# Performance work log

Hardware: AMD Instinct MI355X
Metric: run time of the kernel (lower is better)

## Reference

```python
import jax, jax.numpy as jnp
import numpy as np

N_NODES = 50000


def _mlp(h, W1, b1, W2, b2):
    return jax.nn.relu(h @ W1.T + b1) @ W2.T + b2


def _gine_layer(h, src, dst, e_emb):
    # messages: ReLU(x_src + edge_embedding), summed at destination (PyG GINEConv, eps=0)
    m = jax.nn.relu(h[src] + e_emb)                       # [E, D]
    agg = jax.ops.segment_sum(m, dst, num_segments=N_NODES)
    return h + agg                                         # (1+eps)*x + agg, eps=0


def setup_inputs() -> dict:
    key = jax.random.key(0)
    ks = jax.random.split(key, 20)
    N, E = N_NODES, 800000
    in_dim, hid, edim, n_types = 64, 128, 16, 100
    s = 0.05
    inp = {
        "x": jax.random.normal(ks[0], (N, in_dim), jnp.float32),
        "edge_index": jax.random.randint(ks[1], (2, E), 0, N, jnp.int64),
        "edge_attr": jax.random.normal(ks[2], (E, edim), jnp.float32),
        "edge_weights": jax.random.uniform(ks[3], (E,), jnp.float32),
        # layer 1: edge lin edim->in_dim, node MLP in_dim->hid->hid
        "We1": jax.random.normal(ks[4], (in_dim, edim), jnp.float32) * s,
        "be1": jnp.zeros((in_dim,), jnp.float32),
        "W11": jax.random.normal(ks[5], (hid, in_dim), jnp.float32) * s,
        "b11": jnp.zeros((hid,), jnp.float32),
        "W12": jax.random.normal(ks[6], (hid, hid), jnp.float32) * s,
        "b12": jnp.zeros((hid,), jnp.float32),
        # layer 2: edge lin edim->hid, node MLP hid->hid->hid
        "We2": jax.random.normal(ks[7], (hid, edim), jnp.float32) * s,
        "be2": jnp.zeros((hid,), jnp.float32),
        "W21": jax.random.normal(ks[8], (hid, hid), jnp.float32) * s,
        "b21": jnp.zeros((hid,), jnp.float32),
        "W22": jax.random.normal(ks[9], (hid, hid), jnp.float32) * s,
        "b22": jnp.zeros((hid,), jnp.float32),
        # output head hid -> n_atom_types
        "Wo": jax.random.normal(ks[10], (n_types, hid), jnp.float32) * s,
        "bo": jnp.zeros((n_types,), jnp.float32),
    }
    return inp


def reference(x, edge_index, edge_attr, edge_weights,
              We1, be1, W11, b11, W12, b12,
              We2, be2, W21, b21, W22, b22,
              Wo, bo):
    src, dst = edge_index[0], edge_index[1]
    ea = edge_attr * edge_weights[:, None]                 # per-edge scaling
    # layer 1
    h = _gine_layer(x, src, dst, ea @ We1.T + be1)
    h = jax.nn.relu(_mlp(h, W11, b11, W12, b12))
    # layer 2
    h = _gine_layer(h, src, dst, ea @ We2.T + be2)
    h = jax.nn.relu(_mlp(h, W21, b21, W22, b22))
    return h @ Wo.T + bo
```

## Files before the change

### kernel.cpp

```cpp
#include <hip/hip_runtime.h>

#define N_NODES 50000
#define E_EDGES 800000
#define SCAN_NB 196

__global__ __launch_bounds__(256) void k_hist(
    const int* __restrict__ ei, int* __restrict__ cnt)
{
    const int e = blockIdx.x * 256 + threadIdx.x;
    if (e < E_EDGES) atomicAdd(&cnt[ei[E_EDGES + e]], 1);
}

__global__ __launch_bounds__(256) void k_scan1(
    const int* __restrict__ cnt, int* __restrict__ bsum)
{
    __shared__ int red[256];
    const int tid = threadIdx.x;
    const int i = blockIdx.x * 256 + tid;
    red[tid] = (i < N_NODES) ? cnt[i] : 0;
    __syncthreads();
    for (int off = 128; off > 0; off >>= 1) {
        if (tid < off) red[tid] += red[tid + off];
        __syncthreads();
    }
    if (tid == 0) bsum[blockIdx.x] = red[0];
}

__global__ __launch_bounds__(256) void k_scan2(
    const int* __restrict__ bsum, int* __restrict__ boff)
{
    __shared__ int part[256];
    const int tid = threadIdx.x;
    const int v = (tid < SCAN_NB) ? bsum[tid] : 0;
    part[tid] = v;
    __syncthreads();
    for (int off = 1; off < 256; off <<= 1) {
        const int vv = part[tid];
        const int u = (tid >= off) ? part[tid - off] : 0;
        __syncthreads();
        part[tid] = vv + u;
        __syncthreads();
    }
    if (tid < SCAN_NB) boff[tid] = part[tid] - v;
}

__global__ __launch_bounds__(256) void k_scan3(
    const int* __restrict__ cnt, const int* __restrict__ boff,
    int* __restrict__ rowptr, int* __restrict__ cursor)
{
    __shared__ int part[256];
    const int tid = threadIdx.x;
    const int i = blockIdx.x * 256 + tid;
    const int v = (i < N_NODES) ? cnt[i] : 0;
    part[tid] = v;
    __syncthreads();
    for (int off = 1; off < 256; off <<= 1) {
        const int vv = part[tid];
        const int u = (tid >= off) ? part[tid - off] : 0;
        __syncthreads();
        part[tid] = vv + u;
        __syncthreads();
    }
    const int excl = part[tid] - v + boff[blockIdx.x];
    if (i < N_NODES) { rowptr[i] = excl; cursor[i] = excl; }
    if (i == N_NODES) rowptr[N_NODES] = excl;
}

__global__ __launch_bounds__(256) void k_scatter(
    const int* __restrict__ ei, int* __restrict__ cursor, int2* __restrict__ pairs)
{
    const int e = blockIdx.x * 256 + threadIdx.x;
    if (e < E_EDGES) {
        const int dst = ei[E_EDGES + e];
        const int pos = atomicAdd(&cursor[dst], 1);
        pairs[pos] = make_int2(ei[e], e);
    }
}

__global__ __launch_bounds__(256) void k_prep(
    const int2* __restrict__ pairs, const float* __restrict__ eattr,
    const float* __restrict__ ew, float* __restrict__ eaw, int* __restrict__ srcs)
{
    const int t = blockIdx.x * 256 + threadIdx.x;
    const int pos = t >> 2;
    if (pos >= E_EDGES) return;
    const int q = t & 3;
    const int2 p = pairs[pos];
    if (q == 0) srcs[pos] = p.x;
    const float w = ew[p.y];
    const float4 a = *((const float4*)(eattr + (size_t)p.y * 16) + q);
    *((float4*)(eaw + (size_t)pos * 16) + q) =
        make_float4(a.x * w, a.y * w, a.z * w, a.w * w);
}

__global__ __launch_bounds__(256) void k_wt(
    const float* __restrict__ W11, const float* __restrict__ W12,
    const float* __restrict__ W21, const float* __restrict__ W22,
    const float* __restrict__ Wo,
    const float* __restrict__ We1, const float* __restrict__ We2,
    float* __restrict__ WT)
{
    const int bid = blockIdx.x;
    const int tid = threadIdx.x;
    if (bid < 288) {
        const float* src; int KIN, JOUT, lbase, obase;
        if (bid < 32)       { src = W11; KIN = 64;  JOUT = 128; lbase = 0;   obase = 0; }
        else if (bid < 96)  { src = W12; KIN = 128; JOUT = 128; lbase = 32;  obase = 8192; }
        else if (bid < 160) { src = W21; KIN = 128; JOUT = 128; lbase = 96;  obase = 24576; }
        else if (bid < 224) { src = W22; KIN = 128; JOUT = 128; lbase = 160; obase = 40960; }
        else                { src = Wo;  KIN = 128; JOUT = 100; lbase = 224; obase = 57344; }
        const int idx = (bid - lbase) * 256 + tid;
        const int k = idx >> 7, j = idx & 127;
        WT[obase + idx] = (j < JOUT) ? src[j * KIN + k] : 0.f;
    } else if (bid < 292) {
        const int idx = (bid - 288) * 256 + tid;
        const int k = idx >> 6, d = idx & 63;
        WT[73728 + idx] = We1[d * 16 + k];
    } else {
        const int idx = (bid - 292) * 256 + tid;
        const int k = idx >> 7, d = idx & 127;
        WT[74752 + idx] = We2[d * 16 + k];
    }
}

__global__ __launch_bounds__(256, 4) void k_edge1(
    const int* __restrict__ rp, const int* __restrict__ srcs,
    const float* __restrict__ eaw,
    const float* __restrict__ WeT1, const float* __restrict__ be1,
    const float* __restrict__ x, float* __restrict__ out)
{
    const int lane = threadIdx.x & 63;
    const int node =
        __builtin_amdgcn_readfirstlane(blockIdx.x * 4 + (threadIdx.x >> 6));
    if (node >= N_NODES) return;

    float wr[16];
#pragma unroll
    for (int k = 0; k < 16; ++k) wr[k] = WeT1[k * 64 + lane];
    const float bias = be1[lane];

    const int beg = rp[node], end = rp[node + 1];
    float acc = 0.f;

#pragma unroll 4
    for (int c = beg; c < end; ++c) {
        const int src = srcs[c];
        const float hv = x[(size_t)src * 64 + lane];
        const float* ep = eaw + (size_t)c * 16;
        float d = bias;
#pragma unroll
        for (int k = 0; k < 16; ++k) d = fmaf(ep[k], wr[k], d);
        acc += fmaxf(hv + d, 0.f);
    }
    out[(size_t)node * 64 + lane] = x[(size_t)node * 64 + lane] + acc;
}

__global__ __launch_bounds__(256, 4) void k_edge2(
    const int* __restrict__ rp, const int* __restrict__ srcs,
    const float* __restrict__ eaw,
    const float* __restrict__ WeT2, const float* __restrict__ be2,
    const float* __restrict__ h, float* __restrict__ out)
{
    const int lane = threadIdx.x & 63;
    const int node =
        __builtin_amdgcn_readfirstlane(blockIdx.x * 4 + (threadIdx.x >> 6));
    if (node >= N_NODES) return;

    const int dA = 2 * lane;
    float wrA[16], wrB[16];
#pragma unroll
    for (int k = 0; k < 16; ++k) {
        const float2 w = *(const float2*)(WeT2 + k * 128 + dA);
        wrA[k] = w.x; wrB[k] = w.y;
    }
    const float2 bv = *(const float2*)(be2 + dA);
    const float biasA = bv.x, biasB = bv.y;

    const int beg = rp[node], end = rp[node + 1];
    float accA = 0.f, accB = 0.f;

    const float* hrow = h + dA;

#pragma unroll 4
    for (int c = beg; c < end; ++c) {
        const int src = srcs[c];
        const float2 hv = *(const float2*)(hrow + (size_t)src * 128);
        const float* ep = eaw + (size_t)c * 16;
        float dA_ = biasA, dB_ = biasB;
#pragma unroll
        for (int k = 0; k < 16; ++k) {
            dA_ = fmaf(ep[k], wrA[k], dA_);
            dB_ = fmaf(ep[k], wrB[k], dB_);
        }
        accA += fmaxf(hv.x + dA_, 0.f);
        accB += fmaxf(hv.y + dB_, 0.f);
    }
    const float2 self = *(const float2*)(h + (size_t)node * 128 + dA);
    *(float2*)(out + (size_t)node * 128 + dA) =
        make_float2(self.x + accA, self.y + accB);
}

#define NT 128

template<int KIN, int JOUT, bool RELU>
__global__ __launch_bounds__(256) void k_mlp(
    const float* __restrict__ H, const float* __restrict__ WT,
    const float* __restrict__ b, float* __restrict__ OUT)
{
    extern __shared__ float hT[];
    const int tid  = threadIdx.x;
    const int lane = tid & 63;
    const int wv   = __builtin_amdgcn_readfirstlane(tid >> 6);
    const int j0   = wv * 32;
    const int base = blockIdx.x * NT;

    for (int idx = tid; idx < NT * (KIN / 4); idx += 256) {
        const int q = idx & (KIN / 4 - 1);
        const int n = idx / (KIN / 4);
        const int ng = (base + n < N_NODES) ? (base + n) : (N_NODES - 1);
        const float4 v = *(const float4*)(H + (size_t)ng * KIN + 4 * q);
        hT[(4 * q + 0) * 129 + n] = v.x;
        hT[(4 * q + 1) * 129 + n] = v.y;
        hT[(4 * q + 2) * 129 + n] = v.z;
        hT[(4 * q + 3) * 129 + n] = v.w;
    }
    __syncthreads();

    float acc0[32], acc1[32];
#pragma unroll
    for (int m = 0; m < 32; ++m) { acc0[m] = 0.f; acc1[m] = 0.f; }

    float wc[32];
#pragma unroll
    for (int m = 0; m < 32; ++m) wc[m] = WT[j0 + m];
    float h0 = hT[lane], h1 = hT[lane + 64];

    for (int k = 0; k < KIN - 1; ++k) {
        float wn[32];
#pragma unroll
        for (int m = 0; m < 32; ++m) wn[m] = WT[(k + 1) * 128 + j0 + m];
        const float h0n = hT[(k + 1) * 129 + lane];
        const float h1n = hT[(k + 1) * 129 + lane + 64];
#pragma unroll
        for (int m = 0; m < 32; ++m) {
            acc0[m] = fmaf(h0, wc[m], acc0[m]);
            acc1[m] = fmaf(h1, wc[m], acc1[m]);
        }
#pragma unroll
        for (int m = 0; m < 32; ++m) wc[m] = wn[m];
        h0 = h0n; h1 = h1n;
    }
#pragma unroll
    for (int m = 0; m < 32; ++m) {
        acc0[m] = fmaf(h0, wc[m], acc0[m]);
        acc1[m] = fmaf(h1, wc[m], acc1[m]);
    }

    float bv[32];
#pragma unroll
    for (int m = 0; m < 32; ++m) bv[m] = (j0 + m < JOUT) ? b[j0 + m] : 0.f;

    const int n0 = base + lane, n1 = base + lane + 64;
    if (n0 < N_NODES) {
        float* row = OUT + (size_t)n0 * JOUT;
#pragma unroll
        for (int g = 0; g < 8; ++g) {
            if (j0 + 4 * g < JOUT) {
                float4 v;
                v.x = acc0[4 * g + 0] + bv[4 * g + 0];
                v.y = acc0[4 * g + 1] + bv[4 * g + 1];
                v.z = acc0[4 * g + 2] + bv[4 * g + 2];
                v.w = acc0[4 * g + 3] + bv[4 * g + 3];
                if (RELU) {
                    v.x = fmaxf(v.x, 0.f); v.y = fmaxf(v.y, 0.f);
                    v.z = fmaxf(v.z, 0.f); v.w = fmaxf(v.w, 0.f);
                }
                *(float4*)(row + j0 + 4 * g) = v;
            }
        }
    }
    if (n1 < N_NODES) {
        float* row = OUT + (size_t)n1 * JOUT;
#pragma unroll
        for (int g = 0; g < 8; ++g) {
            if (j0 + 4 * g < JOUT) {
                float4 v;
                v.x = acc1[4 * g + 0] + bv[4 * g + 0];
                v.y = acc1[4 * g + 1] + bv[4 * g + 1];
                v.z = acc1[4 * g + 2] + bv[4 * g + 2];
                v.w = acc1[4 * g + 3] + bv[4 * g + 3];
                if (RELU) {
                    v.x = fmaxf(v.x, 0.f); v.y = fmaxf(v.y, 0.f);
                    v.z = fmaxf(v.z, 0.f); v.w = fmaxf(v.w, 0.f);
                }
                *(float4*)(row + j0 + 4 * g) = v;
            }
        }
    }
}

extern "C" void kernel_launch(void* const* d_in, const int* in_sizes, int n_in,
                              void* d_out, int out_size, void* d_ws, size_t ws_size,
                              hipStream_t stream) {
    const float* x     = (const float*)d_in[0];
    const int*   ei    = (const int*)  d_in[1];
    const float* eattr = (const float*)d_in[2];
    const float* ew    = (const float*)d_in[3];
    const float* We1   = (const float*)d_in[4];
    const float* be1   = (const float*)d_in[5];
    const float* W11   = (const float*)d_in[6];
    const float* b11   = (const float*)d_in[7];
    const float* W12   = (const float*)d_in[8];
    const float* b12   = (const float*)d_in[9];
    const float* We2   = (const float*)d_in[10];
    const float* be2   = (const float*)d_in[11];
    const float* W21   = (const float*)d_in[12];
    const float* b21   = (const float*)d_in[13];
    const float* W22   = (const float*)d_in[14];
    const float* b22   = (const float*)d_in[15];
    const float* Wo    = (const float*)d_in[16];
    const float* bo    = (const float*)d_in[17];
    float* out = (float*)d_out;

    char* ws = (char*)d_ws;
    int*   rowptr = (int*)  (ws + 0);
    int*   cnt    = (int*)  (ws + 204800);
    int*   cursor = (int*)  (ws + 409600);
    int*   srcs   = (int*)  (ws + 204800);
    float* eaw    = (float*)(ws + 3404800);
    float* t1     = (float*)(ws + 54604800);
    int2*  pairs  = (int2*) (ws + 54604800);
    float* h2pre  = (float*)(ws + 80204800);
    float* h1pre  = (float*)(ws + 80204800);
    float* WT     = (float*)(ws + 105804800);
    float* WT11 = WT;
    float* WT12 = WT + 8192;
    float* WT21 = WT + 24576;
    float* WT22 = WT + 40960;
    float* WTo  = WT + 57344;
    float* WeT1 = WT + 73728;
    float* WeT2 = WT + 74752;
    int*   bsum = (int*)(ws + 106116096);
    int*   boff = (int*)(ws + 106117120);

    hipMemsetAsync(cnt, 0, 200000, stream);

    k_wt<<<300, 256, 0, stream>>>(W11, W12, W21, W22, Wo, We1, We2, WT);

    const int EB = (E_EDGES + 255) / 256;
    k_hist<<<EB, 256, 0, stream>>>(ei, cnt);
    k_scan1<<<SCAN_NB, 256, 0, stream>>>(cnt, bsum);
    k_scan2<<<1, 256, 0, stream>>>(bsum, boff);
    k_scan3<<<SCAN_NB, 256, 0, stream>>>(cnt, boff, rowptr, cursor);
    k_scatter<<<EB, 256, 0, stream>>>(ei, cursor, pairs);

    const int PB = (E_EDGES * 4 + 255) / 256;
    k_prep<<<PB, 256, 0, stream>>>(pairs, eattr, ew, eaw, srcs);

    const int NB = (N_NODES + 3) / 4;
    k_edge1<<<NB, 256, 0, stream>>>(rowptr, srcs, eaw, WeT1, be1, x, h1pre);

    const int TILES = (N_NODES + NT - 1) / NT;
    const size_t lds64  = (size_t)(64  * 129) * 4;
    const size_t lds128 = (size_t)(128 * 129) * 4;

    k_mlp<64, 128, true><<<TILES, 256, lds64, stream>>>(h1pre, WT11, b11, t1);
    k_mlp<128, 128, true><<<TILES, 256, lds128, stream>>>(t1, WT12, b12, t1);

    k_edge2<<<NB, 256, 0, stream>>>(rowptr, srcs, eaw, WeT2, be2, t1, h2pre);

    k_mlp<128, 128, true><<<TILES, 256, lds128, stream>>>(h2pre, WT21, b21, h2pre);
    k_mlp<128, 128, true><<<TILES, 256, lds128, stream>>>(h2pre, WT22, b22, h2pre);
    k_mlp<128, 100, false><<<TILES, 256, lds128, stream>>>(h2pre, WTo, bo, out);
}
```

Baseline: 550.7 us.

## Fuse consecutive node MLP layers into single kernels with LDS-resident intermediates

Replaces the five separate per-layer MLP launches with two fused kernels: one runs both layers of the first node MLP, the other runs both layers of the second MLP plus the output head. Intermediate activations stay in LDS, so the global writes and reads of [N,128] tensors between layers go away. Tiles shrink from 128 to 64 nodes per block, with one accumulator set per thread instead of two. That halves weight reuse per global load of WT and changes occupancy.

```diff
diff --git a/kernel.cpp b/kernel.cpp
--- a/kernel.cpp
+++ b/kernel.cpp
@@ -200,99 +200,134 @@
         make_float2(self.x + accA, self.y + accB);
 }
 
-#define NT 128
-
-template<int KIN, int JOUT, bool RELU>
-__global__ __launch_bounds__(256) void k_mlp(
-    const float* __restrict__ H, const float* __restrict__ WT,
-    const float* __restrict__ b, float* __restrict__ OUT)
-{
-    extern __shared__ float hT[];
-    const int tid  = threadIdx.x;
-    const int lane = tid & 63;
-    const int wv   = __builtin_amdgcn_readfirstlane(tid >> 6);
-    const int j0   = wv * 32;
-    const int base = blockIdx.x * NT;
-
-    for (int idx = tid; idx < NT * (KIN / 4); idx += 256) {
+
+template<int KIN>
+__device__ __forceinline__ void gstage(
+    const float* __restrict__ WTb, int j0,
+    const float* S, int lane, float acc[32])
+{
+#pragma unroll
+    for (int m = 0; m < 32; ++m) acc[m] = 0.f;
+    float wA[32], wB[32];
+#pragma unroll
+    for (int m = 0; m < 32; ++m) wA[m] = WTb[j0 + m];
+    float hA = S[lane];
+    for (int k = 0; k < KIN; k += 2) {
+#pragma unroll
+        for (int m = 0; m < 32; ++m) wB[m] = WTb[(k + 1) * 128 + j0 + m];
+        const float hB = S[(k + 1) * 65 + lane];
+#pragma unroll
+        for (int m = 0; m < 32; ++m) acc[m] = fmaf(hA, wA[m], acc[m]);
+        if (k + 2 < KIN) {
+#pragma unroll
+            for (int m = 0; m < 32; ++m) wA[m] = WTb[(k + 2) * 128 + j0 + m];
+            hA = S[(k + 2) * 65 + lane];
+        }
+#pragma unroll
+        for (int m = 0; m < 32; ++m) acc[m] = fmaf(hB, wB[m], acc[m]);
+    }
+}
+
+template<int KIN>
+__device__ __forceinline__ void stage_tile(
+    const float* __restrict__ H, int base, int tid, float* S)
+{
+    for (int idx = tid; idx < 64 * (KIN / 4); idx += 256) {
         const int q = idx & (KIN / 4 - 1);
         const int n = idx / (KIN / 4);
         const int ng = (base + n < N_NODES) ? (base + n) : (N_NODES - 1);
         const float4 v = *(const float4*)(H + (size_t)ng * KIN + 4 * q);
-        hT[(4 * q + 0) * 129 + n] = v.x;
-        hT[(4 * q + 1) * 129 + n] = v.y;
-        hT[(4 * q + 2) * 129 + n] = v.z;
-        hT[(4 * q + 3) * 129 + n] = v.w;
-    }
-    __syncthreads();
-
-    float acc0[32], acc1[32];
-#pragma unroll
-    for (int m = 0; m < 32; ++m) { acc0[m] = 0.f; acc1[m] = 0.f; }
-
-    float wc[32];
-#pragma unroll
-    for (int m = 0; m < 32; ++m) wc[m] = WT[j0 + m];
-    float h0 = hT[lane], h1 = hT[lane + 64];
-
-    for (int k = 0; k < KIN - 1; ++k) {
-        float wn[32];
-#pragma unroll
-        for (int m = 0; m < 32; ++m) wn[m] = WT[(k + 1) * 128 + j0 + m];
-        const float h0n = hT[(k + 1) * 129 + lane];
-        const float h1n = hT[(k + 1) * 129 + lane + 64];
-#pragma unroll
-        for (int m = 0; m < 32; ++m) {
-            acc0[m] = fmaf(h0, wc[m], acc0[m]);
-            acc1[m] = fmaf(h1, wc[m], acc1[m]);
+        S[(4 * q + 0) * 65 + n] = v.x;
+        S[(4 * q + 1) * 65 + n] = v.y;
+        S[(4 * q + 2) * 65 + n] = v.z;
+        S[(4 * q + 3) * 65 + n] = v.w;
+    }
+}
+
+__global__ __launch_bounds__(256) void k_mlp2(
+    const float* __restrict__ H, const float* __restrict__ WT11,
+    const float* __restrict__ b11, const float* __restrict__ WT12,
+    const float* __restrict__ b12, float* __restrict__ OUT)
+{
+    extern __shared__ float lds[];
+    float* A = lds;
+    float* B = lds + 64 * 65;
+    const int tid  = threadIdx.x;
+    const int lane = tid & 63;
+    const int j0   = __builtin_amdgcn_readfirstlane(tid >> 6) * 32;
+    const int base = blockIdx.x * 64;
+
+    stage_tile<64>(H, base, tid, A);
+    __syncthreads();
+
+    float acc[32];
+    gstage<64>(WT11, j0, A, lane, acc);
+#pragma unroll
+    for (int m = 0; m < 32; ++m)
+        B[(j0 + m) * 65 + lane] = fmaxf(acc[m] + b11[j0 + m], 0.f);
+    __syncthreads();
+
+    gstage<128>(WT12, j0, B, lane, acc);
+
+    const int node = base + lane;
+    if (node < N_NODES) {
+        float* row = OUT + (size_t)node * 128 + j0;
+#pragma unroll
+        for (int g = 0; g < 8; ++g) {
+            float4 v;
+            v.x = fmaxf(acc[4 * g + 0] + b12[j0 + 4 * g + 0], 0.f);
+            v.y = fmaxf(acc[4 * g + 1] + b12[j0 + 4 * g + 1], 0.f);
+            v.z = fmaxf(acc[4 * g + 2] + b12[j0 + 4 * g + 2], 0.f);
+            v.w = fmaxf(acc[4 * g + 3] + b12[j0 + 4 * g + 3], 0.f);
+            *(float4*)(row + 4 * g) = v;
         }
-#pragma unroll
-        for (int m = 0; m < 32; ++m) wc[m] = wn[m];
-        h0 = h0n; h1 = h1n;
-    }
-#pragma unroll
-    for (int m = 0; m < 32; ++m) {
-        acc0[m] = fmaf(h0, wc[m], acc0[m]);
-        acc1[m] = fmaf(h1, wc[m], acc1[m]);
-    }
-
-    float bv[32];
-#pragma unroll
-    for (int m = 0; m < 32; ++m) bv[m] = (j0 + m < JOUT) ? b[j0 + m] : 0.f;
-
-    const int n0 = base + lane, n1 = base + lane + 64;
-    if (n0 < N_NODES) {
-        float* row = OUT + (size_t)n0 * JOUT;
+    }
+}
+
+__global__ __launch_bounds__(256) void k_mlp3(
+    const float* __restrict__ H, const float* __restrict__ WT21,
+    const float* __restrict__ b21, const float* __restrict__ WT22,
+    const float* __restrict__ b22, const float* __restrict__ WTo,
+    const float* __restrict__ bo, float* __restrict__ OUT)
+{
+    extern __shared__ float lds[];
+    float* A = lds;
+    float* B = lds + 128 * 65;
+    const int tid  = threadIdx.x;
+    const int lane = tid & 63;
+    const int j0   = __builtin_amdgcn_readfirstlane(tid >> 6) * 32;
+    const int base = blockIdx.x * 64;
+
+    stage_tile<128>(H, base, tid, A);
+    __syncthreads();
+
+    float acc[32];
+    gstage<128>(WT21, j0, A, lane, acc);
+#pragma unroll
+    for (int m = 0; m < 32; ++m)
+        B[(j0 + m) * 65 + lane] = fmaxf(acc[m] + b21[j0 + m], 0.f);
+    __syncthreads();
+
+    gstage<128>(WT22, j0, B, lane, acc);
+    __syncthreads();
+#pragma unroll
+    for (int m = 0; m < 32; ++m)
+        A[(j0 + m) * 65 + lane] = fmaxf(acc[m] + b22[j0 + m], 0.f);
+    __syncthreads();
+
+    gstage<128>(WTo, j0, A, lane, acc);
+
+    const int node = base + lane;
+    if (node < N_NODES) {
+        float* row = OUT + (size_t)node * 100;
 #pragma unroll
         for (int g = 0; g < 8; ++g) {
-            if (j0 + 4 * g < JOUT) {
+            if (j0 + 4 * g < 100) {
                 float4 v;
-                v.x = acc0[4 * g + 0] + bv[4 * g + 0];
-                v.y = acc0[4 * g + 1] + bv[4 * g + 1];
-                v.z = acc0[4 * g + 2] + bv[4 * g + 2];
-                v.w = acc0[4 * g + 3] + bv[4 * g + 3];
-                if (RELU) {
-                    v.x = fmaxf(v.x, 0.f); v.y = fmaxf(v.y, 0.f);
-                    v.z = fmaxf(v.z, 0.f); v.w = fmaxf(v.w, 0.f);
-                }
-                *(float4*)(row + j0 + 4 * g) = v;
-            }
-        }
-    }
-    if (n1 < N_NODES) {
-        float* row = OUT + (size_t)n1 * JOUT;
-#pragma unroll
-        for (int g = 0; g < 8; ++g) {
-            if (j0 + 4 * g < JOUT) {
-                float4 v;
-                v.x = acc1[4 * g + 0] + bv[4 * g + 0];
-                v.y = acc1[4 * g + 1] + bv[4 * g + 1];
-                v.z = acc1[4 * g + 2] + bv[4 * g + 2];
-                v.w = acc1[4 * g + 3] + bv[4 * g + 3];
-                if (RELU) {
-                    v.x = fmaxf(v.x, 0.f); v.y = fmaxf(v.y, 0.f);
-                    v.z = fmaxf(v.z, 0.f); v.w = fmaxf(v.w, 0.f);
-                }
+                v.x = acc[4 * g + 0] + bo[j0 + 4 * g + 0];
+                v.y = acc[4 * g + 1] + bo[j0 + 4 * g + 1];
+                v.z = acc[4 * g + 2] + bo[j0 + 4 * g + 2];
+                v.w = acc[4 * g + 3] + bo[j0 + 4 * g + 3];
                 *(float4*)(row + j0 + 4 * g) = v;
             }
         }
@@ -360,16 +395,13 @@
     const int NB = (N_NODES + 3) / 4;
     k_edge1<<<NB, 256, 0, stream>>>(rowptr, srcs, eaw, WeT1, be1, x, h1pre);
 
-    const int TILES = (N_NODES + NT - 1) / NT;
-    const size_t lds64  = (size_t)(64  * 129) * 4;
-    const size_t lds128 = (size_t)(128 * 129) * 4;
-
-    k_mlp<64, 128, true><<<TILES, 256, lds64, stream>>>(h1pre, WT11, b11, t1);
-    k_mlp<128, 128, true><<<TILES, 256, lds128, stream>>>(t1, WT12, b12, t1);
+    const int MB = (N_NODES + 63) / 64;
+    const size_t ldsA = (size_t)(64 * 65 + 128 * 65) * 4;
+    const size_t ldsB = (size_t)(128 * 65 + 128 * 65) * 4;
+
+    k_mlp2<<<MB, 256, ldsA, stream>>>(h1pre, WT11, b11, WT12, b12, t1);
 
     k_edge2<<<NB, 256, 0, stream>>>(rowptr, srcs, eaw, WeT2, be2, t1, h2pre);
 
-    k_mlp<128, 128, true><<<TILES, 256, lds128, stream>>>(h2pre, WT21, b21, h2pre);
-    k_mlp<128, 128, true><<<TILES, 256, lds128, stream>>>(h2pre, WT22, b22, h2pre);
-    k_mlp<128, 100, false><<<TILES, 256, lds128, stream>>>(h2pre, WTo, bo, out);
-}
+    k_mlp3<<<MB, 256, ldsB, stream>>>(h2pre, WT21, b21, WT22, b22, WTo, bo, out);
+}
```

New measurement: 694.3 us. 1.26x slower.
